# Optimization experiments

Measured on AMD Instinct MI355X. Metric: run time of the kernel, lower is better.

Reference implementation:

```python
import jax, jax.numpy as jnp
import numpy as np

EMB = 1024
HEADS = 16
HEAD_DIM = EMB // HEADS


def setup_inputs() -> dict:
    key = jax.random.key(0)
    ks = jax.random.split(key, 9)
    s = 1.0 / np.sqrt(EMB)
    return {
        "embedding": jax.random.normal(ks[0], (4, 2048, EMB), dtype=jnp.float32),
        "Wq": jax.random.uniform(ks[1], (EMB, EMB), jnp.float32, -s, s),
        "bq": jax.random.uniform(ks[2], (EMB,), jnp.float32, -s, s),
        "Wk": jax.random.uniform(ks[3], (EMB, EMB), jnp.float32, -s, s),
        "bk": jax.random.uniform(ks[4], (EMB,), jnp.float32, -s, s),
        "Wv": jax.random.uniform(ks[5], (EMB, EMB), jnp.float32, -s, s),
        "bv": jax.random.uniform(ks[6], (EMB,), jnp.float32, -s, s),
        "Wo": jax.random.uniform(ks[7], (EMB, EMB), jnp.float32, -s, s),
        "bo": jax.random.uniform(ks[8], (EMB,), jnp.float32, -s, s),
    }


def reference(embedding, Wq, bq, Wk, bk, Wv, bv, Wo, bo):
    B, S, _ = embedding.shape
    # Linear layers (torch Linear: x @ W.T + b)
    Q = embedding @ Wq.T + bq
    K = embedding @ Wk.T + bk
    V = embedding @ Wv.T + bv
    # [B, S, H, Dh] -> [B, H, S, Dh]
    Q = Q.reshape(B, S, HEADS, HEAD_DIM).transpose(0, 2, 1, 3)
    K = K.reshape(B, S, HEADS, HEAD_DIM).transpose(0, 2, 1, 3)
    V = V.reshape(B, S, HEADS, HEAD_DIM).transpose(0, 2, 1, 3)
    scores = jnp.einsum('bhqd,bhkd->bhqk', Q, K) / np.sqrt(HEAD_DIM)
    probs = jax.nn.softmax(scores, axis=-1)
    out = jnp.einsum('bhqk,bhkd->bhqd', probs, V)
    out = out.transpose(0, 2, 1, 3).reshape(B, S, EMB)
    return out @ Wo.T + bo
```

## Files before the change

kernel.cpp:

```cpp
#include <hip/hip_runtime.h>
#include <hip/hip_bf16.h>
#include <cstdint>
#include <cstddef>

typedef __attribute__((ext_vector_type(8))) short bf16x8;
typedef __attribute__((ext_vector_type(4))) float floatx4;

#define BATCH 4
#define SEQ   2048
#define EMBD  1024
#define HEADS 16
#define HD    64
#define NTOK  (BATCH*SEQ)
#define LDT   72
#define QSCALE 0.18033688f

__device__ __forceinline__ short f2bs(float f) {
  union { __hip_bfloat16 b; short s; } u;
  u.b = __float2bfloat16(f);
  return u.s;
}

__device__ __forceinline__ bf16x8 load8f(const float* p) {
  const float4* q = (const float4*)p;
  float4 a = q[0], b = q[1];
  bf16x8 r;
  r[0] = f2bs(a.x); r[1] = f2bs(a.y); r[2] = f2bs(a.z); r[3] = f2bs(a.w);
  r[4] = f2bs(b.x); r[5] = f2bs(b.y); r[6] = f2bs(b.z); r[7] = f2bs(b.w);
  return r;
}

__device__ __forceinline__ unsigned pack_trunc(float lo, float hi) {
  return __builtin_amdgcn_perm(__float_as_uint(hi), __float_as_uint(lo), 0x07060302u);
}

__device__ __forceinline__ void async16(const __hip_bfloat16* g, __hip_bfloat16* l) {
  __builtin_amdgcn_global_load_lds(
      (const __attribute__((address_space(1))) unsigned int*)g,
      (__attribute__((address_space(3))) unsigned int*)l, 16, 0, 0);
}

__global__ __launch_bounds__(256)
void precast(const float* __restrict__ e,  const float* __restrict__ wq,
             const float* __restrict__ wk, const float* __restrict__ wv,
             const float* __restrict__ wo,
             __hip_bfloat16* __restrict__ eB,  __hip_bfloat16* __restrict__ wqB,
             __hip_bfloat16* __restrict__ wkB, __hip_bfloat16* __restrict__ wvB,
             __hip_bfloat16* __restrict__ woB)
{
  int blk = blockIdx.x;
  const float* src; __hip_bfloat16* dst; int base;
  if      (blk < 4096) { src = e;  dst = eB;  base = 0;    }
  else if (blk < 4608) { src = wq; dst = wqB; base = 4096; }
  else if (blk < 5120) { src = wk; dst = wkB; base = 4608; }
  else if (blk < 5632) { src = wv; dst = wvB; base = 5120; }
  else                 { src = wo; dst = woB; base = 5632; }
  size_t idx = ((size_t)(blk - base)*256 + threadIdx.x) * 8;
  *(bf16x8*)(dst + idx) = load8f(src + idx);
}

__device__ __forceinline__ void gemm_bf16_core(
    const __hip_bfloat16* __restrict__ A,
    const __hip_bfloat16* __restrict__ W,
    __hip_bfloat16* sA, __hip_bfloat16* sB,
    floatx4 (&acc)[4][4], int tm, int tn)
{
  const int tid = threadIdx.x;
  const int wid = tid >> 6, lane = tid & 63;
  const int wm = (wid >> 1) * 64, wn = (wid & 1) * 64;
  const int m16 = lane & 15, q = lane >> 4;
  const int lr = lane >> 3;
  const int lc = (lane & 7) ^ lr;

  for (int k0 = 0; k0 < EMBD; k0 += 64) {
    #pragma unroll
    for (int c2 = 0; c2 < 4; ++c2) {
      int c = wid*4 + c2;
      int row = c*8 + lr;
      async16(A + (size_t)(tm + row)*EMBD + k0 + lc*8, sA + c*512);
      async16(W + (size_t)(tn + row)*EMBD + k0 + lc*8, sB + c*512);
    }
    __syncthreads();
    #pragma unroll
    for (int ks = 0; ks < 2; ++ks) {
      bf16x8 af[4], bfr[4];
      #pragma unroll
      for (int i = 0; i < 4; ++i)
        af[i] = *(const bf16x8*)&sA[(wm + i*16 + m16)*64 + ((ks*4 + q) ^ (m16 & 7))*8];
      #pragma unroll
      for (int j = 0; j < 4; ++j)
        bfr[j] = *(const bf16x8*)&sB[(wn + j*16 + m16)*64 + ((ks*4 + q) ^ (m16 & 7))*8];
      #pragma unroll
      for (int i = 0; i < 4; ++i)
        #pragma unroll
        for (int j = 0; j < 4; ++j)
          acc[i][j] = __builtin_amdgcn_mfma_f32_16x16x32_bf16(af[i], bfr[j], acc[i][j], 0, 0, 0);
    }
    __syncthreads();
  }
}

__global__ __launch_bounds__(256)
void gemm_qkv(const __hip_bfloat16* __restrict__ A,
              const __hip_bfloat16* __restrict__ W0, const float* __restrict__ b0, __hip_bfloat16* __restrict__ C0,
              const __hip_bfloat16* __restrict__ W1, const float* __restrict__ b1, __hip_bfloat16* __restrict__ C1,
              const __hip_bfloat16* __restrict__ W2, const float* __restrict__ b2, __hip_bfloat16* __restrict__ C2)
{
  __shared__ __hip_bfloat16 sA[128*64];
  __shared__ __hip_bfloat16 sB[128*64];
  const int z = blockIdx.z;
  const __hip_bfloat16* W = (z == 0) ? W0 : (z == 1) ? W1 : W2;
  const float* bias       = (z == 0) ? b0 : (z == 1) ? b1 : b2;
  __hip_bfloat16* C       = (z == 0) ? C0 : (z == 1) ? C1 : C2;

  const int tm = blockIdx.x * 128, tn = blockIdx.y * 128;
  floatx4 acc[4][4] = {};
  gemm_bf16_core(A, W, sA, sB, acc, tm, tn);

  const int tid = threadIdx.x, wid = tid >> 6, lane = tid & 63;
  const int wm = (wid >> 1) * 64, wn = (wid & 1) * 64;
  const int m16 = lane & 15, q = lane >> 4;

  if (z < 2) {
    const float sc = (z == 0) ? QSCALE : 1.0f;
    #pragma unroll
    for (int i = 0; i < 4; ++i)
      #pragma unroll
      for (int j = 0; j < 4; ++j)
        #pragma unroll
        for (int r = 0; r < 4; ++r) {
          int gm = tm + wm + i*16 + q*4 + r;
          int gn = tn + wn + j*16 + m16;
          float v = (acc[i][j][r] + bias[gn]) * sc;
          int b = gm >> 11, s = gm & (SEQ - 1);
          int h = gn >> 6,  d = gn & (HD - 1);
          size_t bh = (size_t)(b*HEADS + h);
          C[(bh*SEQ + s)*HD + d] = __float2bfloat16(v);
        }
  } else {
    #pragma unroll
    for (int i = 0; i < 4; ++i)
      #pragma unroll
      for (int j = 0; j < 4; ++j) {
        int gm0 = tm + wm + i*16 + q*4;
        int gn  = tn + wn + j*16 + m16;
        float bv = bias[gn];
        int b = gm0 >> 11, s0 = gm0 & (SEQ - 1);
        int h = gn >> 6,  d = gn & (HD - 1);
        size_t bh = (size_t)(b*HEADS + h);
        short4 pk;
        pk.x = f2bs(acc[i][j][0] + bv);
        pk.y = f2bs(acc[i][j][1] + bv);
        pk.z = f2bs(acc[i][j][2] + bv);
        pk.w = f2bs(acc[i][j][3] + bv);
        *(short4*)&C[(bh*HD + d)*SEQ + s0] = pk;
      }
  }
}

__global__ __launch_bounds__(256)
void gemm_outp(const __hip_bfloat16* __restrict__ A,
               const __hip_bfloat16* __restrict__ W, const float* __restrict__ bias,
               float* __restrict__ C)
{
  __shared__ __hip_bfloat16 sA[128*64];
  __shared__ __hip_bfloat16 sB[128*64];
  const int tm = blockIdx.x * 128, tn = blockIdx.y * 128;
  floatx4 acc[4][4] = {};
  gemm_bf16_core(A, W, sA, sB, acc, tm, tn);
  const int tid = threadIdx.x, wid = tid >> 6, lane = tid & 63;
  const int wm = (wid >> 1) * 64, wn = (wid & 1) * 64;
  const int m16 = lane & 15, q = lane >> 4;
  #pragma unroll
  for (int i = 0; i < 4; ++i)
    #pragma unroll
    for (int j = 0; j < 4; ++j)
      #pragma unroll
      for (int r = 0; r < 4; ++r) {
        int gm = tm + wm + i*16 + q*4 + r;
        int gn = tn + wn + j*16 + m16;
        C[(size_t)gm*EMBD + gn] = acc[i][j][r] + bias[gn];
      }
}

__global__ __launch_bounds__(256)
void attn_fused(const __hip_bfloat16* __restrict__ Q,
                const __hip_bfloat16* __restrict__ Km,
                const __hip_bfloat16* __restrict__ Vt,
                __hip_bfloat16* __restrict__ O)
{
  __shared__ __hip_bfloat16 sQ[64*64], sK[64*64], sVT[64*64];
  __shared__ __hip_bfloat16 sP[4][16*LDT];
  const int tid = threadIdx.x, wid = tid >> 6, lane = tid & 63;
  const int m16 = lane & 15, g = lane >> 4;
  const int lr = lane >> 3;
  const int lc = (lane & 7) ^ lr;
  const int qt = blockIdx.x & 31;
  const int bh = blockIdx.x >> 5;
  const int b = bh >> 4, h = bh & (HEADS - 1);

  const __hip_bfloat16* Qb = Q  + ((size_t)bh*SEQ + qt*64) * HD;
  const __hip_bfloat16* Kb = Km + (size_t)bh*SEQ*HD;
  const __hip_bfloat16* Vb = Vt + (size_t)bh*HD*SEQ;

  #pragma unroll
  for (int c2 = 0; c2 < 2; ++c2) {
    int c = wid*2 + c2;
    async16(Qb + (size_t)(c*8 + lr)*HD + lc*8, sQ + c*512);
  }
  __syncthreads();

  bf16x8 qf[2];
  #pragma unroll
  for (int ks = 0; ks < 2; ++ks)
    qf[ks] = *(const bf16x8*)&sQ[(wid*16 + m16)*64 + ((ks*4 + g) ^ (m16 & 7))*8];

  bf16x8 onesf;
  #pragma unroll
  for (int i = 0; i < 8; ++i) onesf[i] = (short)0x3F80;

  floatx4 o_acc[4] = {};
  floatx4 lacc = {};

  for (int kt = 0; kt < SEQ/64; ++kt) {
    #pragma unroll
    for (int c2 = 0; c2 < 2; ++c2) {
      int c = wid*2 + c2;
      int row = c*8 + lr;
      async16(Kb + (size_t)(kt*64 + row)*HD + lc*8, sK + c*512);
      async16(Vb + (size_t)row*SEQ + kt*64 + lc*8, sVT + c*512);
    }
    __syncthreads();

    floatx4 st[4] = {};
    #pragma unroll
    for (int ks = 0; ks < 2; ++ks) {
      #pragma unroll
      for (int nt = 0; nt < 4; ++nt) {
        bf16x8 kf = *(const bf16x8*)&sK[(nt*16 + m16)*64 + ((ks*4 + g) ^ (m16 & 7))*8];
        st[nt] = __builtin_amdgcn_mfma_f32_16x16x32_bf16(kf, qf[ks], st[nt], 0, 0, 0);
      }
    }

    #pragma unroll
    for (int nt = 0; nt < 4; ++nt) {
      float p0 = __builtin_amdgcn_exp2f(st[nt][0]);
      float p1 = __builtin_amdgcn_exp2f(st[nt][1]);
      float p2 = __builtin_amdgcn_exp2f(st[nt][2]);
      float p3 = __builtin_amdgcn_exp2f(st[nt][3]);
      uint2 u;
      u.x = pack_trunc(p0, p1);
      u.y = pack_trunc(p2, p3);
      *(uint2*)&sP[wid][m16*LDT + nt*16 + g*4] = u;
    }

    #pragma unroll
    for (int ks = 0; ks < 2; ++ks) {
      bf16x8 af = *(const bf16x8*)&sP[wid][m16*LDT + ks*32 + g*8];
      lacc = __builtin_amdgcn_mfma_f32_16x16x32_bf16(af, onesf, lacc, 0, 0, 0);
      #pragma unroll
      for (int dt = 0; dt < 4; ++dt) {
        bf16x8 bfr = *(const bf16x8*)&sVT[(dt*16 + m16)*64 + ((ks*4 + g) ^ (m16 & 7))*8];
        o_acc[dt] = __builtin_amdgcn_mfma_f32_16x16x32_bf16(af, bfr, o_acc[dt], 0, 0, 0);
      }
    }
    __syncthreads();
  }

  float inv[4];
  #pragma unroll
  for (int r = 0; r < 4; ++r) inv[r] = 1.0f / lacc[r];

  #pragma unroll
  for (int dt = 0; dt < 4; ++dt)
    #pragma unroll
    for (int r = 0; r < 4; ++r) {
      int s = qt*64 + wid*16 + g*4 + r;
      int d = dt*16 + m16;
      float v = o_acc[dt][r] * inv[r];
      O[((size_t)(b*SEQ + s))*EMBD + h*HD + d] = __float2bfloat16(v);
    }
}

extern "C" void kernel_launch(void* const* d_in, const int* in_sizes, int n_in,
                              void* d_out, int out_size, void* d_ws, size_t ws_size,
                              hipStream_t stream) {
  const float* emb = (const float*)d_in[0];
  const float* Wq  = (const float*)d_in[1];
  const float* bq  = (const float*)d_in[2];
  const float* Wk  = (const float*)d_in[3];
  const float* bk  = (const float*)d_in[4];
  const float* Wv  = (const float*)d_in[5];
  const float* bv  = (const float*)d_in[6];
  const float* Wo  = (const float*)d_in[7];
  const float* bo  = (const float*)d_in[8];

  const size_t T = (size_t)NTOK*EMBD;
  const size_t WN = (size_t)EMBD*EMBD;
  __hip_bfloat16* Qw  = (__hip_bfloat16*)d_ws;
  __hip_bfloat16* Kw  = Qw + T;
  __hip_bfloat16* Vw  = Kw + T;
  __hip_bfloat16* Aw  = Vw + T;
  __hip_bfloat16* embB = Aw;
  __hip_bfloat16* WqB = Aw + T;
  __hip_bfloat16* WkB = WqB + WN;
  __hip_bfloat16* WvB = WkB + WN;
  __hip_bfloat16* WoB = WvB + WN;
  float* Ob = (float*)d_out;

  precast<<<dim3(6144), 256, 0, stream>>>(emb, Wq, Wk, Wv, Wo,
                                          embB, WqB, WkB, WvB, WoB);

  dim3 gq(NTOK/128, EMBD/128, 3);
  gemm_qkv<<<gq, 256, 0, stream>>>(embB, WqB, bq, Qw, WkB, bk, Kw, WvB, bv, Vw);

  attn_fused<<<dim3(64*32), 256, 0, stream>>>(Qw, Kw, Vw, Aw);

  dim3 go(NTOK/128, EMBD/128);
  gemm_outp<<<go, 256, 0, stream>>>(Aw, WoB, bo, Ob);
}
```

Measured before the change: 294.7 us.

## Double-buffer K/V tiles and process two query tiles per attention block

The attention kernel now handles 128 query rows per block (two 64-row sub-tiles per wave set), so each K/V tile loaded into shared memory is reused twice, halving K/V traffic and the grid size. K/V staging is double-buffered so the next tile's async loads overlap with the current tile's MFMA work, and V fragments are hoisted into registers once per tile. Q is loaded straight from global memory into registers. The cost is higher register pressure and fewer blocks, which may reduce occupancy.

```diff
diff --git a/kernel.cpp b/kernel.cpp
--- a/kernel.cpp
+++ b/kernel.cpp
@@ -189,97 +189,107 @@
                 const __hip_bfloat16* __restrict__ Vt,
                 __hip_bfloat16* __restrict__ O)
 {
-  __shared__ __hip_bfloat16 sQ[64*64], sK[64*64], sVT[64*64];
+  __shared__ __hip_bfloat16 sK[2][64*64], sVT[2][64*64];
   __shared__ __hip_bfloat16 sP[4][16*LDT];
   const int tid = threadIdx.x, wid = tid >> 6, lane = tid & 63;
   const int m16 = lane & 15, g = lane >> 4;
   const int lr = lane >> 3;
   const int lc = (lane & 7) ^ lr;
-  const int qt = blockIdx.x & 31;
-  const int bh = blockIdx.x >> 5;
+  const int qt = blockIdx.x & 15;
+  const int bh = blockIdx.x >> 4;
   const int b = bh >> 4, h = bh & (HEADS - 1);
 
-  const __hip_bfloat16* Qb = Q  + ((size_t)bh*SEQ + qt*64) * HD;
+  const __hip_bfloat16* Qb = Q  + ((size_t)bh*SEQ + qt*128) * HD;
   const __hip_bfloat16* Kb = Km + (size_t)bh*SEQ*HD;
   const __hip_bfloat16* Vb = Vt + (size_t)bh*HD*SEQ;
 
+  bf16x8 qf[2][2];
   #pragma unroll
-  for (int c2 = 0; c2 < 2; ++c2) {
-    int c = wid*2 + c2;
-    async16(Qb + (size_t)(c*8 + lr)*HD + lc*8, sQ + c*512);
-  }
-  __syncthreads();
-
-  bf16x8 qf[2];
-  #pragma unroll
-  for (int ks = 0; ks < 2; ++ks)
-    qf[ks] = *(const bf16x8*)&sQ[(wid*16 + m16)*64 + ((ks*4 + g) ^ (m16 & 7))*8];
+  for (int u = 0; u < 2; ++u)
+    #pragma unroll
+    for (int ks = 0; ks < 2; ++ks)
+      qf[u][ks] = *(const bf16x8*)(Qb + (size_t)(u*64 + wid*16 + m16)*HD + ks*32 + g*8);
 
   bf16x8 onesf;
   #pragma unroll
   for (int i = 0; i < 8; ++i) onesf[i] = (short)0x3F80;
 
-  floatx4 o_acc[4] = {};
-  floatx4 lacc = {};
+  floatx4 o_acc[2][4] = {};
+  floatx4 lacc[2] = {};
+
+  #define STAGE(KT, BUF)                                                     \
+    { int _c = wid*2;                                                        \
+      _Pragma("unroll")                                                      \
+      for (int c2 = 0; c2 < 2; ++c2) {                                       \
+        int c = _c + c2, row = c*8 + lr;                                     \
+        async16(Kb + (size_t)((KT)*64 + row)*HD + lc*8, sK[BUF] + c*512);    \
+        async16(Vb + (size_t)row*SEQ + (KT)*64 + lc*8,  sVT[BUF] + c*512);   \
+      } }
+
+  STAGE(0, 0)
 
   for (int kt = 0; kt < SEQ/64; ++kt) {
-    #pragma unroll
-    for (int c2 = 0; c2 < 2; ++c2) {
-      int c = wid*2 + c2;
-      int row = c*8 + lr;
-      async16(Kb + (size_t)(kt*64 + row)*HD + lc*8, sK + c*512);
-      async16(Vb + (size_t)row*SEQ + kt*64 + lc*8, sVT + c*512);
+    const int cur = kt & 1;
+    __syncthreads();
+    if (kt < SEQ/64 - 1) STAGE(kt + 1, cur ^ 1)
+
+    bf16x8 vtf[2][4];
+    #pragma unroll
+    for (int ks = 0; ks < 2; ++ks)
+      #pragma unroll
+      for (int dt = 0; dt < 4; ++dt)
+        vtf[ks][dt] = *(const bf16x8*)&sVT[cur][(dt*16 + m16)*64 + ((ks*4 + g) ^ (m16 & 7))*8];
+
+    floatx4 st[2][4] = {};
+    #pragma unroll
+    for (int ks = 0; ks < 2; ++ks) {
+      #pragma unroll
+      for (int nt = 0; nt < 4; ++nt) {
+        bf16x8 kf = *(const bf16x8*)&sK[cur][(nt*16 + m16)*64 + ((ks*4 + g) ^ (m16 & 7))*8];
+        st[0][nt] = __builtin_amdgcn_mfma_f32_16x16x32_bf16(kf, qf[0][ks], st[0][nt], 0, 0, 0);
+        st[1][nt] = __builtin_amdgcn_mfma_f32_16x16x32_bf16(kf, qf[1][ks], st[1][nt], 0, 0, 0);
+      }
     }
-    __syncthreads();
-
-    floatx4 st[4] = {};
-    #pragma unroll
-    for (int ks = 0; ks < 2; ++ks) {
+
+    #pragma unroll
+    for (int u = 0; u < 2; ++u) {
       #pragma unroll
       for (int nt = 0; nt < 4; ++nt) {
-        bf16x8 kf = *(const bf16x8*)&sK[(nt*16 + m16)*64 + ((ks*4 + g) ^ (m16 & 7))*8];
-        st[nt] = __builtin_amdgcn_mfma_f32_16x16x32_bf16(kf, qf[ks], st[nt], 0, 0, 0);
+        float p0 = __builtin_amdgcn_exp2f(st[u][nt][0]);
+        float p1 = __builtin_amdgcn_exp2f(st[u][nt][1]);
+        float p2 = __builtin_amdgcn_exp2f(st[u][nt][2]);
+        float p3 = __builtin_amdgcn_exp2f(st[u][nt][3]);
+        uint2 pu;
+        pu.x = pack_trunc(p0, p1);
+        pu.y = pack_trunc(p2, p3);
+        *(uint2*)&sP[wid][m16*LDT + nt*16 + g*4] = pu;
+      }
+      #pragma unroll
+      for (int ks = 0; ks < 2; ++ks) {
+        bf16x8 af = *(const bf16x8*)&sP[wid][m16*LDT + ks*32 + g*8];
+        lacc[u] = __builtin_amdgcn_mfma_f32_16x16x32_bf16(af, onesf, lacc[u], 0, 0, 0);
+        #pragma unroll
+        for (int dt = 0; dt < 4; ++dt)
+          o_acc[u][dt] = __builtin_amdgcn_mfma_f32_16x16x32_bf16(af, vtf[ks][dt], o_acc[u][dt], 0, 0, 0);
       }
     }
-
-    #pragma unroll
-    for (int nt = 0; nt < 4; ++nt) {
-      float p0 = __builtin_amdgcn_exp2f(st[nt][0]);
-      float p1 = __builtin_amdgcn_exp2f(st[nt][1]);
-      float p2 = __builtin_amdgcn_exp2f(st[nt][2]);
-      float p3 = __builtin_amdgcn_exp2f(st[nt][3]);
-      uint2 u;
-      u.x = pack_trunc(p0, p1);
-      u.y = pack_trunc(p2, p3);
-      *(uint2*)&sP[wid][m16*LDT + nt*16 + g*4] = u;
-    }
-
-    #pragma unroll
-    for (int ks = 0; ks < 2; ++ks) {
-      bf16x8 af = *(const bf16x8*)&sP[wid][m16*LDT + ks*32 + g*8];
-      lacc = __builtin_amdgcn_mfma_f32_16x16x32_bf16(af, onesf, lacc, 0, 0, 0);
-      #pragma unroll
-      for (int dt = 0; dt < 4; ++dt) {
-        bf16x8 bfr = *(const bf16x8*)&sVT[(dt*16 + m16)*64 + ((ks*4 + g) ^ (m16 & 7))*8];
-        o_acc[dt] = __builtin_amdgcn_mfma_f32_16x16x32_bf16(af, bfr, o_acc[dt], 0, 0, 0);
-      }
-    }
-    __syncthreads();
   }
 
-  float inv[4];
   #pragma unroll
-  for (int r = 0; r < 4; ++r) inv[r] = 1.0f / lacc[r];
-
-  #pragma unroll
-  for (int dt = 0; dt < 4; ++dt)
-    #pragma unroll
-    for (int r = 0; r < 4; ++r) {
-      int s = qt*64 + wid*16 + g*4 + r;
-      int d = dt*16 + m16;
-      float v = o_acc[dt][r] * inv[r];
-      O[((size_t)(b*SEQ + s))*EMBD + h*HD + d] = __float2bfloat16(v);
-    }
+  for (int u = 0; u < 2; ++u) {
+    float inv[4];
+    #pragma unroll
+    for (int r = 0; r < 4; ++r) inv[r] = 1.0f / lacc[u][r];
+    #pragma unroll
+    for (int dt = 0; dt < 4; ++dt)
+      #pragma unroll
+      for (int r = 0; r < 4; ++r) {
+        int s = qt*128 + u*64 + wid*16 + g*4 + r;
+        int d = dt*16 + m16;
+        float v = o_acc[u][dt][r] * inv[r];
+        O[((size_t)(b*SEQ + s))*EMBD + h*HD + d] = __float2bfloat16(v);
+      }
+  }
 }
 
 extern "C" void kernel_launch(void* const* d_in, const int* in_sizes, int n_in,
@@ -314,7 +324,7 @@
   dim3 gq(NTOK/128, EMBD/128, 3);
   gemm_qkv<<<gq, 256, 0, stream>>>(embB, WqB, bq, Qw, WkB, bk, Kw, WvB, bv, Vw);
 
-  attn_fused<<<dim3(64*32), 256, 0, stream>>>(Qw, Kw, Vw, Aw);
+  attn_fused<<<dim3(64*16), 256, 0, stream>>>(Qw, Kw, Vw, Aw);
 
   dim3 go(NTOK/128, EMBD/128);
   gemm_outp<<<go, 256, 0, stream>>>(Aw, WoB, bo, Ob);
```

New measurement: 296.1 us. No clear change (+0.5%).
